# Kernel tuning notes

Hardware: AMD Instinct MI355X
Metric: run time of the kernel (lower is better)

The kernel has to match this reference:

```python
import jax, jax.numpy as jnp
import numpy as np
import math

B, S, D, H = 4, 2048, 1024, 16
HD = D // H  # head_dim = 64


def setup_inputs() -> dict:
    key = jax.random.key(0)
    ks = jax.random.split(key, 7)
    s = 0.02
    return {
        "q": jax.random.normal(ks[0], (B, S, D), jnp.float32),
        "k": jax.random.normal(ks[1], (B, S, D), jnp.float32),
        "v": jax.random.normal(ks[2], (B, S, D), jnp.float32),
        "wq": jax.random.normal(ks[3], (D, D), jnp.float32) * s,
        "wk": jax.random.normal(ks[4], (D, D), jnp.float32) * s,
        "wv": jax.random.normal(ks[5], (D, D), jnp.float32) * s,
        "wo": jax.random.normal(ks[6], (D, D), jnp.float32) * s,
    }


def reference(q, k, v, wq, wk, wv, wo):
    # Linear (no bias): y = x @ W.T, W is (out, in)
    xq = jnp.einsum('bsd,ed->bse', q, wq).reshape(B, S, H, HD).transpose(0, 2, 1, 3)
    xk = jnp.einsum('bsd,ed->bse', k, wk).reshape(B, S, H, HD).transpose(0, 2, 1, 3)
    xv = jnp.einsum('bsd,ed->bse', v, wv).reshape(B, S, H, HD).transpose(0, 2, 1, 3)
    scores = jnp.einsum('bhqd,bhkd->bhqk', xq, xk) / math.sqrt(HD)  # [B,H,S,S]
    causal = jnp.tril(jnp.ones((S, S), dtype=bool))
    scores = jnp.where(causal[None, None], scores, jnp.float32(-jnp.inf))
    probs = jax.nn.softmax(scores, axis=-1)  # dropout p=0 -> identity
    out = jnp.einsum('bhqk,bhkd->bhqd', probs, xv)  # [B,H,S,HD]
    out = out.transpose(0, 2, 1, 3).reshape(B, S, D)
    return jnp.einsum('bsd,ed->bse', out, wo)
```

## Files before the change

kernel.cpp:

```cpp
#include <hip/hip_runtime.h>

#define SS 2048
#define DD 1024
#define HH 16
#define HD 64
#define MM 8192

typedef unsigned short ushort_t;
typedef __attribute__((ext_vector_type(8))) short short8;
typedef __attribute__((ext_vector_type(4))) float f32x4;
typedef __attribute__((ext_vector_type(4))) unsigned short us4;

__device__ __forceinline__ ushort_t f2bf(float f) {
    union { float f; unsigned u; } x; x.f = f;
    unsigned r = x.u + 0x7fffu + ((x.u >> 16) & 1u);
    return (ushort_t)(r >> 16);
}
__device__ __forceinline__ float bf2f(ushort_t h) {
    union { unsigned u; float f; } x; x.u = ((unsigned)h) << 16; return x.f;
}
__device__ __forceinline__ unsigned pack_bf2(float a, float b) {
    union { float f; unsigned u; } x, y; x.f = a; y.f = b;
    return __builtin_amdgcn_perm(y.u, x.u, 0x07060302u);
}

__device__ __forceinline__ void async16(const void* g, void* l) {
    __builtin_amdgcn_global_load_lds(
        (const __attribute__((address_space(1))) unsigned int*)g,
        (__attribute__((address_space(3))) unsigned int*)l, 16, 0, 0);
}

__global__ void cvt_w(const float* __restrict__ wq, const float* __restrict__ wk,
                      const float* __restrict__ wv, const float* __restrict__ wo,
                      ushort_t* __restrict__ dst) {
    int i = (blockIdx.x * 256 + threadIdx.x) * 4;
    int w = i >> 20, j = i & 1048575;
    const float* src = (w == 0) ? wq : (w == 1) ? wk : (w == 2) ? wv : wo;
    float4 f = *(const float4*)(src + j);
    us4 o; o.x = f2bf(f.x); o.y = f2bf(f.y); o.z = f2bf(f.z); o.w = f2bf(f.w);
    *(us4*)(dst + i) = o;
}

__device__ __forceinline__ void epi_scatter(f32x4 acc[4][4], int m0, int n0,
                                            int mode, void* Yv) {
    int tid = threadIdx.x;
    int w = tid >> 6, lane = tid & 63;
    int l16 = lane & 15, quad = lane >> 4;
    int wm = (w >> 1) * 64, wn = (w & 1) * 64;
    #pragma unroll
    for (int mt = 0; mt < 4; ++mt) {
        #pragma unroll
        for (int r = 0; r < 4; ++r) {
            int row = m0 + wm + mt * 16 + quad * 4 + r;
            #pragma unroll
            for (int nt = 0; nt < 4; ++nt) {
                int col = n0 + wn + nt * 16 + l16;
                float vf = acc[mt][nt][r];
                if (mode == 2) {
                    ((float*)Yv)[(size_t)row * DD + col] = vf;
                } else {
                    ushort_t vh = f2bf(vf);
                    int b = row >> 11, s = row & 2047;
                    int h = col >> 6,  hd = col & 63;
                    if (mode == 0) {
                        ((ushort_t*)Yv)[(((size_t)b * HH + h) * SS + s) * HD + hd] = vh;
                    } else {
                        int sp = (s & ~63) | (((s & 15) << 2) | ((s >> 4) & 3));
                        ((ushort_t*)Yv)[(((size_t)b * HH + h) * HD + hd) * SS + sp] = vh;
                    }
                }
            }
        }
    }
}

__global__ __launch_bounds__(256) void proj3f(const float* __restrict__ q,
                                              const float* __restrict__ k,
                                              const float* __restrict__ v,
                                              const ushort_t* __restrict__ Wall,
                                              ushort_t* __restrict__ xq,
                                              ushort_t* __restrict__ xk,
                                              ushort_t* __restrict__ xvT) {
    __shared__ __align__(16) ushort_t As[2][128 * 32];
    __shared__ __align__(16) ushort_t Bs[2][128 * 32];
    int tid = threadIdx.x;
    int w = tid >> 6, lane = tid & 63;
    int l16 = lane & 15, quad = lane >> 4;
    int mat   = (int)(blockIdx.x >> 9);
    int inner = (int)(blockIdx.x & 511);
    int m0 = (inner & 63) * 128;
    int n0 = (inner >> 6) * 128;
    const float*    A  = (mat == 0) ? q : (mat == 1) ? k : v;
    const ushort_t* Bw = Wall + ((size_t)mat << 20);
    int wm = (w >> 1) * 64, wn = (w & 1) * 64;

    f32x4 acc[4][4];
    #pragma unroll
    for (int i = 0; i < 4; ++i)
        #pragma unroll
        for (int j = 0; j < 4; ++j) acc[i][j] = (f32x4){0.f, 0.f, 0.f, 0.f};

    int g0 = w * 64 + lane, r0 = g0 >> 2, j0 = ((g0 & 3) ^ (r0 & 3)) * 8;
    int g1 = g0 + 256,      r1 = g1 >> 2, j1 = ((g1 & 3) ^ (r1 & 3)) * 8;
    int ar0 = tid >> 2,         ac0 = tid & 3;
    int ar1 = (tid + 256) >> 2, ac1 = (tid + 256) & 3;
    int aw0 = ar0 * 32 + ((ac0 ^ (ar0 & 3)) * 8);
    int aw1 = ar1 * 32 + ((ac1 ^ (ar1 & 3)) * 8);
    const float* Arow0 = A + (size_t)(m0 + ar0) * DD + ac0 * 8;
    const float* Arow1 = A + (size_t)(m0 + ar1) * DD + ac1 * 8;
    int swA = (quad ^ (l16 & 3)) * 8;

    {
        float4 f0 = *(const float4*)(Arow0), f1 = *(const float4*)(Arow0 + 4);
        float4 f2 = *(const float4*)(Arow1), f3 = *(const float4*)(Arow1 + 4);
        async16(Bw + (size_t)(n0 + r0) * DD + j0, &Bs[0][(size_t)(w * 64) * 8]);
        async16(Bw + (size_t)(n0 + r1) * DD + j1, &Bs[0][(size_t)(256 + w * 64) * 8]);
        uint4 p0 = { pack_bf2(f0.x, f0.y), pack_bf2(f0.z, f0.w),
                     pack_bf2(f1.x, f1.y), pack_bf2(f1.z, f1.w) };
        uint4 p1 = { pack_bf2(f2.x, f2.y), pack_bf2(f2.z, f2.w),
                     pack_bf2(f3.x, f3.y), pack_bf2(f3.z, f3.w) };
        *(uint4*)&As[0][aw0] = p0;
        *(uint4*)&As[0][aw1] = p1;
    }

    for (int kk = 0; kk < 32; ++kk) {
        int c = kk & 1;
        __syncthreads();
        bool pf = (kk < 31);
        float4 f0, f1, f2, f3;
        if (pf) {
            int k1 = (kk + 1) * 32;
            f0 = *(const float4*)(Arow0 + k1); f1 = *(const float4*)(Arow0 + k1 + 4);
            f2 = *(const float4*)(Arow1 + k1); f3 = *(const float4*)(Arow1 + k1 + 4);
            async16(Bw + (size_t)(n0 + r0) * DD + k1 + j0, &Bs[c ^ 1][(size_t)(w * 64) * 8]);
            async16(Bw + (size_t)(n0 + r1) * DD + k1 + j1, &Bs[c ^ 1][(size_t)(256 + w * 64) * 8]);
        }

        short8 af[4], bfr[4];
        #pragma unroll
        for (int t = 0; t < 4; ++t) {
            af[t]  = *(const short8*)&As[c][(wm + t * 16 + l16) * 32 + swA];
            bfr[t] = *(const short8*)&Bs[c][(wn + t * 16 + l16) * 32 + swA];
        }
        #pragma unroll
        for (int mt = 0; mt < 4; ++mt)
            #pragma unroll
            for (int nt = 0; nt < 4; ++nt)
                acc[mt][nt] = __builtin_amdgcn_mfma_f32_16x16x32_bf16(af[mt], bfr[nt], acc[mt][nt], 0, 0, 0);

        if (pf) {
            uint4 p0 = { pack_bf2(f0.x, f0.y), pack_bf2(f0.z, f0.w),
                         pack_bf2(f1.x, f1.y), pack_bf2(f1.z, f1.w) };
            uint4 p1 = { pack_bf2(f2.x, f2.y), pack_bf2(f2.z, f2.w),
                         pack_bf2(f3.x, f3.y), pack_bf2(f3.z, f3.w) };
            *(uint4*)&As[c ^ 1][aw0] = p0;
            *(uint4*)&As[c ^ 1][aw1] = p1;
        }
    }

    void* Y = (mat == 0) ? (void*)xq : (mat == 1) ? (void*)xk : (void*)xvT;
    epi_scatter(acc, m0, n0, (mat == 2) ? 1 : 0, Y);
}

__global__ __launch_bounds__(256) void out_gemm(const ushort_t* __restrict__ Abf,
                                                const ushort_t* __restrict__ Bw,
                                                float* __restrict__ Y) {
    __shared__ __align__(16) ushort_t As[2][128 * 32];
    __shared__ __align__(16) ushort_t Bs[2][128 * 32];
    int tid = threadIdx.x;
    int w = tid >> 6, lane = tid & 63;
    int l16 = lane & 15, quad = lane >> 4;
    int m0 = (int)(blockIdx.x & 63) * 128;
    int n0 = (int)(blockIdx.x >> 6) * 128;
    int wm = (w >> 1) * 64, wn = (w & 1) * 64;

    f32x4 acc[4][4];
    #pragma unroll
    for (int i = 0; i < 4; ++i)
        #pragma unroll
        for (int j = 0; j < 4; ++j) acc[i][j] = (f32x4){0.f, 0.f, 0.f, 0.f};

    int g0 = w * 64 + lane, r0 = g0 >> 2, j0 = ((g0 & 3) ^ (r0 & 3)) * 8;
    int g1 = g0 + 256,      r1 = g1 >> 2, j1 = ((g1 & 3) ^ (r1 & 3)) * 8;
    int swA = (quad ^ (l16 & 3)) * 8;

    async16(Abf + (size_t)(m0 + r0) * DD + j0, &As[0][(size_t)(w * 64) * 8]);
    async16(Abf + (size_t)(m0 + r1) * DD + j1, &As[0][(size_t)(256 + w * 64) * 8]);
    async16(Bw  + (size_t)(n0 + r0) * DD + j0, &Bs[0][(size_t)(w * 64) * 8]);
    async16(Bw  + (size_t)(n0 + r1) * DD + j1, &Bs[0][(size_t)(256 + w * 64) * 8]);

    for (int kk = 0; kk < 32; ++kk) {
        int c = kk & 1;
        __syncthreads();
        if (kk < 31) {
            int k1 = (kk + 1) * 32;
            async16(Abf + (size_t)(m0 + r0) * DD + k1 + j0, &As[c ^ 1][(size_t)(w * 64) * 8]);
            async16(Abf + (size_t)(m0 + r1) * DD + k1 + j1, &As[c ^ 1][(size_t)(256 + w * 64) * 8]);
            async16(Bw  + (size_t)(n0 + r0) * DD + k1 + j0, &Bs[c ^ 1][(size_t)(w * 64) * 8]);
            async16(Bw  + (size_t)(n0 + r1) * DD + k1 + j1, &Bs[c ^ 1][(size_t)(256 + w * 64) * 8]);
        }
        short8 af[4], bfr[4];
        #pragma unroll
        for (int t = 0; t < 4; ++t) {
            af[t]  = *(const short8*)&As[c][(wm + t * 16 + l16) * 32 + swA];
            bfr[t] = *(const short8*)&Bs[c][(wn + t * 16 + l16) * 32 + swA];
        }
        #pragma unroll
        for (int mt = 0; mt < 4; ++mt)
            #pragma unroll
            for (int nt = 0; nt < 4; ++nt)
                acc[mt][nt] = __builtin_amdgcn_mfma_f32_16x16x32_bf16(af[mt], bfr[nt], acc[mt][nt], 0, 0, 0);
    }
    epi_scatter(acc, m0, n0, 2, Y);
}

__global__ __launch_bounds__(256) void attn_kernel(const ushort_t* __restrict__ xq,
                                                   const ushort_t* __restrict__ xk,
                                                   const ushort_t* __restrict__ xvT,
                                                   ushort_t* __restrict__ ao) {
    __shared__ __align__(16) ushort_t Ksm[2][64 * 64];
    __shared__ __align__(16) ushort_t Vsm[2][64 * 64];
    __shared__ __align__(16) ushort_t Psm[4][16 * 72];

    int tid = threadIdx.x;
    int w = tid >> 6, lane = tid & 63;
    int l16 = lane & 15, quad = lane >> 4;
    int bh = blockIdx.x & 63;
    int p  = blockIdx.x >> 6;
    int b = bh >> 4, h = bh & 15;

    const ushort_t* Q  = xq  + (size_t)bh * SS * HD;
    const ushort_t* K  = xk  + (size_t)bh * SS * HD;
    const ushort_t* VT = xvT + (size_t)bh * HD * SS;

    int g0 = w * 64 + lane, r0 = g0 >> 3, j0 = ((g0 & 7) ^ (r0 & 7)) * 8;
    int g1 = g0 + 256,      r1 = g1 >> 3, j1 = ((g1 & 7) ^ (r1 & 7)) * 8;

    short8 ones;
    #pragma unroll
    for (int i = 0; i < 8; ++i) ones[i] = (short)0x3F80;

    const float CS = 0.125f * 1.44269504f;

    for (int ph = 0; ph < 2; ++ph) {
        int qt = ph ? (31 - p) : p;
        int qb = qt * 64;
        int qmin = qb + w * 16;

        short8 aq[2];
        #pragma unroll
        for (int kc = 0; kc < 2; ++kc) {
            short8 t = *(const short8*)(Q + (size_t)(qmin + l16) * HD + kc * 32 + quad * 8);
            #pragma unroll
            for (int i = 0; i < 8; ++i)
                t[i] = (short)f2bf(bf2f((ushort_t)t[i]) * CS);
            aq[kc] = t;
        }

        f32x4 o[4];
        #pragma unroll
        for (int dt = 0; dt < 4; ++dt) o[dt] = (f32x4){0.f, 0.f, 0.f, 0.f};
        f32x4 lacc = (f32x4){0.f, 0.f, 0.f, 0.f};

        __syncthreads();
        async16(K  + (size_t)r0 * HD + j0, &Ksm[0][(size_t)(w * 64) * 8]);
        async16(K  + (size_t)r1 * HD + j1, &Ksm[0][(size_t)(256 + w * 64) * 8]);
        async16(VT + (size_t)r0 * SS + j0, &Vsm[0][(size_t)(w * 64) * 8]);
        async16(VT + (size_t)r1 * SS + j1, &Vsm[0][(size_t)(256 + w * 64) * 8]);

        for (int kt = 0; kt <= qt; ++kt) {
            int kb = kt * 64;
            int c = kt & 1;
            __syncthreads();
            if (kt < qt) {
                int kb1 = kb + 64;
                async16(K  + (size_t)(kb1 + r0) * HD + j0, &Ksm[c ^ 1][(size_t)(w * 64) * 8]);
                async16(K  + (size_t)(kb1 + r1) * HD + j1, &Ksm[c ^ 1][(size_t)(256 + w * 64) * 8]);
                async16(VT + (size_t)r0 * SS + kb1 + j0, &Vsm[c ^ 1][(size_t)(w * 64) * 8]);
                async16(VT + (size_t)r1 * SS + kb1 + j1, &Vsm[c ^ 1][(size_t)(256 + w * 64) * 8]);
            }

            f32x4 sc[4];
            #pragma unroll
            for (int nt = 0; nt < 4; ++nt) {
                int row = nt * 16 + l16;
                short8 bk0 = *(const short8*)&Ksm[c][row * 64 + ((0 + quad) ^ (l16 & 7)) * 8];
                short8 bk1 = *(const short8*)&Ksm[c][row * 64 + ((4 + quad) ^ (l16 & 7)) * 8];
                f32x4 cc = (f32x4){0.f, 0.f, 0.f, 0.f};
                cc = __builtin_amdgcn_mfma_f32_16x16x32_bf16(aq[0], bk0, cc, 0, 0, 0);
                cc = __builtin_amdgcn_mfma_f32_16x16x32_bf16(aq[1], bk1, cc, 0, 0, 0);
                sc[nt] = cc;
            }

            bool msk = (kt == qt);
            #pragma unroll
            for (int r = 0; r < 4; ++r) {
                float e0, e1, e2, e3;
                if (msk) {
                    int qg = qmin + quad * 4 + r;
                    e0 = (kb +  0 + l16 <= qg) ? __builtin_amdgcn_exp2f(sc[0][r]) : 0.f;
                    e1 = (kb + 16 + l16 <= qg) ? __builtin_amdgcn_exp2f(sc[1][r]) : 0.f;
                    e2 = (kb + 32 + l16 <= qg) ? __builtin_amdgcn_exp2f(sc[2][r]) : 0.f;
                    e3 = (kb + 48 + l16 <= qg) ? __builtin_amdgcn_exp2f(sc[3][r]) : 0.f;
                } else {
                    e0 = __builtin_amdgcn_exp2f(sc[0][r]);
                    e1 = __builtin_amdgcn_exp2f(sc[1][r]);
                    e2 = __builtin_amdgcn_exp2f(sc[2][r]);
                    e3 = __builtin_amdgcn_exp2f(sc[3][r]);
                }
                uint2 pk = { pack_bf2(e0, e1), pack_bf2(e2, e3) };
                *(uint2*)&Psm[w][(quad * 4 + r) * 72 + l16 * 4] = pk;
            }

            asm volatile("s_waitcnt lgkmcnt(0)" ::: "memory");

            #pragma unroll
            for (int kc = 0; kc < 2; ++kc) {
                short8 ap = *(const short8*)&Psm[w][l16 * 72 + kc * 32 + quad * 8];
                lacc = __builtin_amdgcn_mfma_f32_16x16x32_bf16(ap, ones, lacc, 0, 0, 0);
                #pragma unroll
                for (int dt = 0; dt < 4; ++dt) {
                    int row = dt * 16 + l16;
                    short8 bv = *(const short8*)&Vsm[c][row * 64 + ((kc * 4 + quad) ^ (l16 & 7)) * 8];
                    o[dt] = __builtin_amdgcn_mfma_f32_16x16x32_bf16(ap, bv, o[dt], 0, 0, 0);
                }
            }
        }

        #pragma unroll
        for (int r = 0; r < 4; ++r) {
            float inv = 1.0f / lacc[r];
            int qg = qmin + quad * 4 + r;
            #pragma unroll
            for (int dt = 0; dt < 4; ++dt)
                ao[((size_t)(b * SS + qg)) * DD + h * HD + dt * 16 + l16] = f2bf(o[dt][r] * inv);
        }
    }
}

extern "C" void kernel_launch(void* const* d_in, const int* in_sizes, int n_in,
                              void* d_out, int out_size, void* d_ws, size_t ws_size,
                              hipStream_t stream) {
    const float* q  = (const float*)d_in[0];
    const float* k  = (const float*)d_in[1];
    const float* v  = (const float*)d_in[2];
    const float* wq = (const float*)d_in[3];
    const float* wk = (const float*)d_in[4];
    const float* wv = (const float*)d_in[5];
    const float* wo = (const float*)d_in[6];
    float* out = (float*)d_out;

    ushort_t* wbf = (ushort_t*)d_ws;
    ushort_t* xq  = wbf + 4194304ull;
    ushort_t* xk  = xq  + 8388608ull;
    ushort_t* xvT = xk  + 8388608ull;
    ushort_t* ao  = xvT + 8388608ull;

    cvt_w<<<4096, 256, 0, stream>>>(wq, wk, wv, wo, wbf);
    proj3f<<<1536, 256, 0, stream>>>(q, k, v, wbf, xq, xk, xvT);
    attn_kernel<<<1024, 256, 0, stream>>>(xq, xk, xvT, ao);
    out_gemm<<<512, 256, 0, stream>>>(ao, wbf + 3145728ull, out);
}
```

Measured before the change: 345.1 us.

## Pre-convert activations to bf16 and stream projection A tiles via async LDS loads

Input activations q, k and v are now converted to bf16 in a combined conversion kernel alongside the weights, using scratch space in the output buffer and the attention-output workspace. The projection GEMM then loads A tiles with async global-to-LDS copies, as it already did for B. This removes the register-staged fp32 loads and the in-loop packing from the GEMM. In exchange it adds a full extra read and write of the activations in a separate pass.

```diff
diff --git a/kernel.cpp b/kernel.cpp
--- a/kernel.cpp
+++ b/kernel.cpp
@@ -10,6 +10,7 @@
 typedef __attribute__((ext_vector_type(8))) short short8;
 typedef __attribute__((ext_vector_type(4))) float f32x4;
 typedef __attribute__((ext_vector_type(4))) unsigned short us4;
+typedef __attribute__((ext_vector_type(8))) unsigned short us8;
 
 __device__ __forceinline__ ushort_t f2bf(float f) {
     union { float f; unsigned u; } x; x.f = f;
@@ -30,15 +31,31 @@
         (__attribute__((address_space(3))) unsigned int*)l, 16, 0, 0);
 }
 
-__global__ void cvt_w(const float* __restrict__ wq, const float* __restrict__ wk,
-                      const float* __restrict__ wv, const float* __restrict__ wo,
-                      ushort_t* __restrict__ dst) {
-    int i = (blockIdx.x * 256 + threadIdx.x) * 4;
-    int w = i >> 20, j = i & 1048575;
-    const float* src = (w == 0) ? wq : (w == 1) ? wk : (w == 2) ? wv : wo;
-    float4 f = *(const float4*)(src + j);
-    us4 o; o.x = f2bf(f.x); o.y = f2bf(f.y); o.z = f2bf(f.z); o.w = f2bf(f.w);
-    *(us4*)(dst + i) = o;
+__global__ void cvt_all(const float* __restrict__ q, const float* __restrict__ k,
+                        const float* __restrict__ v, const float* __restrict__ wq,
+                        const float* __restrict__ wk, const float* __restrict__ wv,
+                        const float* __restrict__ wo, ushort_t* __restrict__ qbf,
+                        ushort_t* __restrict__ kbf, ushort_t* __restrict__ vbf,
+                        ushort_t* __restrict__ wbf) {
+    long i = ((long)blockIdx.x * 256 + threadIdx.x) * 8;
+    const float* src; ushort_t* dst;
+    if (i < (3l << 23)) {
+        int s = (int)(i >> 23);
+        long off = i & ((1l << 23) - 1);
+        src = ((s == 0) ? q : (s == 1) ? k : v) + off;
+        dst = ((s == 0) ? qbf : (s == 1) ? kbf : vbf) + off;
+    } else {
+        long j = i - (3l << 23);
+        int s = (int)(j >> 20);
+        src = ((s == 0) ? wq : (s == 1) ? wk : (s == 2) ? wv : wo) + (j & 1048575);
+        dst = wbf + j;
+    }
+    float4 f0 = *(const float4*)src;
+    float4 f1 = *(const float4*)(src + 4);
+    us8 o;
+    o[0] = f2bf(f0.x); o[1] = f2bf(f0.y); o[2] = f2bf(f0.z); o[3] = f2bf(f0.w);
+    o[4] = f2bf(f1.x); o[5] = f2bf(f1.y); o[6] = f2bf(f1.z); o[7] = f2bf(f1.w);
+    *(us8*)dst = o;
 }
 
 __device__ __forceinline__ void epi_scatter(f32x4 acc[4][4], int m0, int n0,
@@ -74,9 +91,9 @@
     }
 }
 
-__global__ __launch_bounds__(256) void proj3f(const float* __restrict__ q,
-                                              const float* __restrict__ k,
-                                              const float* __restrict__ v,
+__global__ __launch_bounds__(256) void proj3f(const ushort_t* __restrict__ qbf,
+                                              const ushort_t* __restrict__ kbf,
+                                              const ushort_t* __restrict__ vbf,
                                               const ushort_t* __restrict__ Wall,
                                               ushort_t* __restrict__ xq,
                                               ushort_t* __restrict__ xk,
@@ -90,7 +107,7 @@
     int inner = (int)(blockIdx.x & 511);
     int m0 = (inner & 63) * 128;
     int n0 = (inner >> 6) * 128;
-    const float*    A  = (mat == 0) ? q : (mat == 1) ? k : v;
+    const ushort_t* A  = (mat == 0) ? qbf : (mat == 1) ? kbf : vbf;
     const ushort_t* Bw = Wall + ((size_t)mat << 20);
     int wm = (w >> 1) * 64, wn = (w & 1) * 64;
 
@@ -102,40 +119,23 @@
 
     int g0 = w * 64 + lane, r0 = g0 >> 2, j0 = ((g0 & 3) ^ (r0 & 3)) * 8;
     int g1 = g0 + 256,      r1 = g1 >> 2, j1 = ((g1 & 3) ^ (r1 & 3)) * 8;
-    int ar0 = tid >> 2,         ac0 = tid & 3;
-    int ar1 = (tid + 256) >> 2, ac1 = (tid + 256) & 3;
-    int aw0 = ar0 * 32 + ((ac0 ^ (ar0 & 3)) * 8);
-    int aw1 = ar1 * 32 + ((ac1 ^ (ar1 & 3)) * 8);
-    const float* Arow0 = A + (size_t)(m0 + ar0) * DD + ac0 * 8;
-    const float* Arow1 = A + (size_t)(m0 + ar1) * DD + ac1 * 8;
     int swA = (quad ^ (l16 & 3)) * 8;
 
-    {
-        float4 f0 = *(const float4*)(Arow0), f1 = *(const float4*)(Arow0 + 4);
-        float4 f2 = *(const float4*)(Arow1), f3 = *(const float4*)(Arow1 + 4);
-        async16(Bw + (size_t)(n0 + r0) * DD + j0, &Bs[0][(size_t)(w * 64) * 8]);
-        async16(Bw + (size_t)(n0 + r1) * DD + j1, &Bs[0][(size_t)(256 + w * 64) * 8]);
-        uint4 p0 = { pack_bf2(f0.x, f0.y), pack_bf2(f0.z, f0.w),
-                     pack_bf2(f1.x, f1.y), pack_bf2(f1.z, f1.w) };
-        uint4 p1 = { pack_bf2(f2.x, f2.y), pack_bf2(f2.z, f2.w),
-                     pack_bf2(f3.x, f3.y), pack_bf2(f3.z, f3.w) };
-        *(uint4*)&As[0][aw0] = p0;
-        *(uint4*)&As[0][aw1] = p1;
-    }
+    async16(A  + (size_t)(m0 + r0) * DD + j0, &As[0][(size_t)(w * 64) * 8]);
+    async16(A  + (size_t)(m0 + r1) * DD + j1, &As[0][(size_t)(256 + w * 64) * 8]);
+    async16(Bw + (size_t)(n0 + r0) * DD + j0, &Bs[0][(size_t)(w * 64) * 8]);
+    async16(Bw + (size_t)(n0 + r1) * DD + j1, &Bs[0][(size_t)(256 + w * 64) * 8]);
 
     for (int kk = 0; kk < 32; ++kk) {
         int c = kk & 1;
         __syncthreads();
-        bool pf = (kk < 31);
-        float4 f0, f1, f2, f3;
-        if (pf) {
+        if (kk < 31) {
             int k1 = (kk + 1) * 32;
-            f0 = *(const float4*)(Arow0 + k1); f1 = *(const float4*)(Arow0 + k1 + 4);
-            f2 = *(const float4*)(Arow1 + k1); f3 = *(const float4*)(Arow1 + k1 + 4);
+            async16(A  + (size_t)(m0 + r0) * DD + k1 + j0, &As[c ^ 1][(size_t)(w * 64) * 8]);
+            async16(A  + (size_t)(m0 + r1) * DD + k1 + j1, &As[c ^ 1][(size_t)(256 + w * 64) * 8]);
             async16(Bw + (size_t)(n0 + r0) * DD + k1 + j0, &Bs[c ^ 1][(size_t)(w * 64) * 8]);
             async16(Bw + (size_t)(n0 + r1) * DD + k1 + j1, &Bs[c ^ 1][(size_t)(256 + w * 64) * 8]);
         }
-
         short8 af[4], bfr[4];
         #pragma unroll
         for (int t = 0; t < 4; ++t) {
@@ -147,15 +147,6 @@
             #pragma unroll
             for (int nt = 0; nt < 4; ++nt)
                 acc[mt][nt] = __builtin_amdgcn_mfma_f32_16x16x32_bf16(af[mt], bfr[nt], acc[mt][nt], 0, 0, 0);
-
-        if (pf) {
-            uint4 p0 = { pack_bf2(f0.x, f0.y), pack_bf2(f0.z, f0.w),
-                         pack_bf2(f1.x, f1.y), pack_bf2(f1.z, f1.w) };
-            uint4 p1 = { pack_bf2(f2.x, f2.y), pack_bf2(f2.z, f2.w),
-                         pack_bf2(f3.x, f3.y), pack_bf2(f3.z, f3.w) };
-            *(uint4*)&As[c ^ 1][aw0] = p0;
-            *(uint4*)&As[c ^ 1][aw1] = p1;
-        }
     }
 
     void* Y = (mat == 0) ? (void*)xq : (mat == 1) ? (void*)xk : (void*)xvT;
@@ -355,9 +346,12 @@
     ushort_t* xk  = xq  + 8388608ull;
     ushort_t* xvT = xk  + 8388608ull;
     ushort_t* ao  = xvT + 8388608ull;
-
-    cvt_w<<<4096, 256, 0, stream>>>(wq, wk, wv, wo, wbf);
-    proj3f<<<1536, 256, 0, stream>>>(q, k, v, wbf, xq, xk, xvT);
+    ushort_t* vbf = ao;
+    ushort_t* qbf = (ushort_t*)d_out;
+    ushort_t* kbf = qbf + 8388608ull;
+
+    cvt_all<<<14336, 256, 0, stream>>>(q, k, v, wq, wk, wv, wo, qbf, kbf, vbf, wbf);
+    proj3f<<<1536, 256, 0, stream>>>(qbf, kbf, vbf, wbf, xq, xk, xvT);
     attn_kernel<<<1024, 256, 0, stream>>>(xq, xk, xvT, ao);
     out_gemm<<<512, 256, 0, stream>>>(ao, wbf + 3145728ull, out);
 }
```

Result: no change. 342.7 us (-0.7%).
